# Kernel optimization log

Measured on AMD Instinct MI355X. Metric: run time of the kernel, lower is better.

The kernel has to match this reference:

```python
import jax, jax.numpy as jnp
from jax import lax
import numpy as np

N_X, N_U, N_Y, HID = 8, 2, 2, 64
T, B = 2048, 1024
SCALE = 0.02  # small weights keep the 2048-step recurrence stable


def setup_inputs() -> dict:
    key = jax.random.key(0)
    ks = jax.random.split(key, 12)
    rn = lambda k, shp: SCALE * jax.random.normal(k, shp, dtype=jnp.float32)
    return {
        "u": jax.random.normal(ks[0], (T, B, N_U), dtype=jnp.float32),
        "y": jax.random.normal(ks[1], (T, B, N_Y), dtype=jnp.float32),
        # f_xu MLP: [x;u] -> 64 -> tanh -> n_x
        "Wf1": rn(ks[2], (N_X + N_U, HID)), "bf1": jnp.zeros((HID,), jnp.float32),
        "Wf2": rn(ks[3], (HID, N_X)),       "bf2": jnp.zeros((N_X,), jnp.float32),
        # g_x: linear n_x -> n_y
        "Wg": rn(ks[4], (N_X, N_Y)),        "bg": jnp.zeros((N_Y,), jnp.float32),
        # gain net: n_x -> 64 -> tanh -> n_x*n_y
        "Wk1": rn(ks[5], (N_X, HID)),       "bk1": jnp.zeros((HID,), jnp.float32),
        "Wk2": rn(ks[6], (HID, N_X * N_Y)), "bk2": jnp.zeros((N_X * N_Y,), jnp.float32),
    }


def reference(u, y, Wf1, bf1, Wf2, bf2, Wg, bg, Wk1, bk1, Wk2, bk2):
    b = u.shape[1]

    def step(x, uy):  # x: [B, n_x]
        u_t, y_t = uy
        y_hat = x @ Wg + bg                                   # [B, n_y]
        K = (jnp.tanh(x @ Wk1 + bk1) @ Wk2 + bk2).reshape(b, N_X, N_Y)
        e = y_hat - y_t                                        # [B, n_y]
        dx = jnp.tanh(jnp.concatenate([x, u_t], -1) @ Wf1 + bf1) @ Wf2 + bf2
        x_new = x + dx + jnp.einsum("bxy,by->bx", K, e)
        return x_new, None

    x0 = jnp.zeros((b, N_X), dtype=u.dtype)
    x_last, _ = lax.scan(step, x0, (u, y))
    return x_last
```

## Files before the change

kernel.cpp:

```cpp
#include <hip/hip_runtime.h>


#define T_STEPS 2048
#define B_SZ    1024
#define NX      8
#define HID     64

typedef float v2f __attribute__((ext_vector_type(2)));

__device__ __forceinline__ v2f pk_fma(v2f a, v2f b, v2f c) {
  v2f d;
  asm("v_pk_fma_f32 %0, %1, %2, %3" : "=v"(d) : "v"(a), "v"(b), "v"(c));
  return d;
}
__device__ __forceinline__ void pk_fma_acc(v2f& acc, v2f a, v2f b) {
  asm("v_pk_fma_f32 %0, %1, %2, %0" : "+v"(acc) : "v"(a), "v"(b));
}
__device__ __forceinline__ v2f pk_fma_s0lo(v2f a, v2f b, v2f c) {
  v2f d;
  asm("v_pk_fma_f32 %0, %1, %2, %3 op_sel:[0,0,0] op_sel_hi:[0,1,1]"
      : "=v"(d) : "v"(a), "v"(b), "v"(c));
  return d;
}
__device__ __forceinline__ v2f pk_fma_s0hi(v2f a, v2f b, v2f c) {
  v2f d;
  asm("v_pk_fma_f32 %0, %1, %2, %3 op_sel:[1,0,0] op_sel_hi:[1,1,1]"
      : "=v"(d) : "v"(a), "v"(b), "v"(c));
  return d;
}
__device__ __forceinline__ void pk_fma_acc_s1lo(v2f& acc, v2f a, v2f b) {
  asm("v_pk_fma_f32 %0, %1, %2, %0 op_sel:[0,0,0] op_sel_hi:[1,0,1]"
      : "+v"(acc) : "v"(a), "v"(b));
}
__device__ __forceinline__ void pk_fma_acc_s1hi(v2f& acc, v2f a, v2f b) {
  asm("v_pk_fma_f32 %0, %1, %2, %0 op_sel:[0,1,0] op_sel_hi:[1,1,1]"
      : "+v"(acc) : "v"(a), "v"(b));
}

__device__ __forceinline__ v2f tanh_pair(float pa, float pb) {
  v2f r;
  r[0] = __builtin_amdgcn_rcpf(__builtin_amdgcn_exp2f(pa) + 1.0f);
  r[1] = __builtin_amdgcn_rcpf(__builtin_amdgcn_exp2f(pb) + 1.0f);
  v2f h;
  h[0] = fmaf(-2.0f, r[0], 1.0f);
  h[1] = fmaf(-2.0f, r[1], 1.0f);
  return h;
}

template <int CTRL, int RMASK>
__device__ __forceinline__ float dpp_add(float acc) {
  int moved = __builtin_amdgcn_update_dpp(0, __float_as_int(acc), CTRL, RMASK, 0xf, true);
  return acc + __int_as_float(moved);
}

__device__ __forceinline__ float half_reduce(float c) {
  c = dpp_add<0x111, 0xf>(c);
  c = dpp_add<0x112, 0xf>(c);
  c = dpp_add<0x114, 0xf>(c);
  c = dpp_add<0x118, 0xf>(c);
  c = dpp_add<0x142, 0xa>(c);
  return c;
}

__device__ __forceinline__ void swap32(float& a, float& b) {
  asm("v_permlane32_swap_b32 %0, %1" : "+v"(a), "+v"(b));
}

__device__ __forceinline__ float rlf(float v, int lane) {
  return __int_as_float(__builtin_amdgcn_readlane(__float_as_int(v), lane));
}

__global__ __launch_bounds__(64, 1) void luen_kernel(
    const float* __restrict__ u, const float* __restrict__ y,
    const float* __restrict__ Wf1, const float* __restrict__ bf1,
    const float* __restrict__ Wf2, const float* __restrict__ bf2,
    const float* __restrict__ Wg, const float* __restrict__ bg,
    const float* __restrict__ Wk1, const float* __restrict__ bk1,
    const float* __restrict__ Wk2, const float* __restrict__ bk2,
    float* __restrict__ out) {
  const int eb = blockIdx.x;
  const int h  = threadIdx.x;

  const float TS = 2.885390081777927f;
  const float INV64 = 1.0f / 64.0f;

  v2f wf1p[5];
#pragma unroll
  for (int p = 0; p < 5; ++p)
    wf1p[p] = v2f{TS * Wf1[(2 * p) * HID + h], TS * Wf1[(2 * p + 1) * HID + h]};
  v2f wk1p[4];
#pragma unroll
  for (int p = 0; p < 4; ++p)
    wk1p[p] = v2f{TS * Wk1[(2 * p) * HID + h], TS * Wk1[(2 * p + 1) * HID + h]};

  v2f wf2p[4], bf2sp[4];
#pragma unroll
  for (int p = 0; p < 4; ++p) {
    wf2p[p]  = v2f{Wf2[h * NX + 2 * p], Wf2[h * NX + 2 * p + 1]};
    bf2sp[p] = v2f{INV64 * bf2[2 * p], INV64 * bf2[2 * p + 1]};
  }
  v2f wk2e[4], wk2o[4], bk2se[4], bk2so[4];
#pragma unroll
  for (int p = 0; p < 4; ++p) {
    const float* r = Wk2 + h * (NX * 2);
    wk2e[p]  = v2f{r[4 * p], r[4 * p + 2]};
    wk2o[p]  = v2f{r[4 * p + 1], r[4 * p + 3]};
    bk2se[p] = v2f{INV64 * bk2[4 * p], INV64 * bk2[4 * p + 2]};
    bk2so[p] = v2f{INV64 * bk2[4 * p + 1], INV64 * bk2[4 * p + 3]};
  }
  v2f wgc0[4], wgc1[4];
#pragma unroll
  for (int p = 0; p < 4; ++p) {
    wgc0[p] = v2f{Wg[4 * p], Wg[4 * p + 2]};
    wgc1[p] = v2f{Wg[4 * p + 1], Wg[4 * p + 3]};
  }
  const v2f a0i = v2f{bg[0], 0.0f};
  const v2f a1i = v2f{bg[1], 0.0f};
  const v2f pfi = v2f{TS * bf1[h], 0.0f};
  const v2f pki = v2f{TS * bk1[h], 0.0f};

  float probe = (h < 32) ? 0.0f : 1.0f;
  float zf = 0.0f;
  swap32(probe, zf);
  const bool dir1 = __builtin_amdgcn_readlane(__float_as_int(probe), 32) != 0;
  const int laneA = dir1 ? 63 : 31;
  const int laneB = dir1 ? 31 : 63;

  const v2f* __restrict__ pu = reinterpret_cast<const v2f*>(u) + eb;
  const v2f* __restrict__ py = reinterpret_cast<const v2f*>(y) + eb;
  const int STR = B_SZ;

  v2f x2[4];
#pragma unroll
  for (int p = 0; p < 4; ++p) x2[p] = v2f{0.0f, 0.0f};

  v2f Au[4], Ay[4], Bu[4], By[4];

#define LOADG(SET_u, SET_y)                          \
  {                                                  \
    SET_u[0] = pu[0 * STR]; SET_u[1] = pu[1 * STR];  \
    SET_u[2] = pu[2 * STR]; SET_u[3] = pu[3 * STR];  \
    SET_y[0] = py[0 * STR]; SET_y[1] = py[1 * STR];  \
    SET_y[2] = py[2 * STR]; SET_y[3] = py[3 * STR];  \
    pu += 4 * STR; py += 4 * STR;                    \
  }

#define STEP(CU_, CY_)                                                        \
  {                                                                           \
    const v2f cu = (CU_);                                                     \
    const v2f cy = (CY_);                                                     \
                                    \
    v2f a0 = pk_fma(x2[0], wgc0[0], a0i);                                     \
    v2f a1 = pk_fma(x2[0], wgc1[0], a1i);                                     \
    pk_fma_acc(a0, x2[1], wgc0[1]); pk_fma_acc(a1, x2[1], wgc1[1]);           \
    pk_fma_acc(a0, x2[2], wgc0[2]); pk_fma_acc(a1, x2[2], wgc1[2]);           \
    pk_fma_acc(a0, x2[3], wgc0[3]); pk_fma_acc(a1, x2[3], wgc1[3]);           \
    v2f ep;                                                                   \
    ep[0] = a0[0] + a0[1] - cy[0];                                            \
    ep[1] = a1[0] + a1[1] - cy[1];                                            \
                   \
    v2f pf = pk_fma(x2[0], wf1p[0], pfi);                                     \
    pk_fma_acc(pf, x2[1], wf1p[1]);                                           \
    pk_fma_acc(pf, x2[2], wf1p[2]);                                           \
    pk_fma_acc(pf, x2[3], wf1p[3]);                                           \
    pk_fma_acc(pf, cu, wf1p[4]);                                              \
    v2f pkv = pk_fma(x2[0], wk1p[0], pki);                                    \
    pk_fma_acc(pkv, x2[1], wk1p[1]);                                          \
    pk_fma_acc(pkv, x2[2], wk1p[2]);                                          \
    pk_fma_acc(pkv, x2[3], wk1p[3]);                                          \
    const v2f hp = tanh_pair(pf[0] + pf[1], pkv[0] + pkv[1]);                 \
                       \
    float c0, c1, c2, c3, c4, c5, c6, c7;                                     \
    {                                                                         \
      v2f t0 = pk_fma_s0hi(hp, wk2e[0], bk2se[0]);                            \
      v2f t1 = pk_fma_s0hi(hp, wk2o[0], bk2so[0]);                            \
      v2f cp = pk_fma_s0lo(hp, wf2p[0], bf2sp[0]);                            \
      pk_fma_acc_s1lo(cp, t0, ep);                                            \
      pk_fma_acc_s1hi(cp, t1, ep);                                            \
      c0 = cp[0]; c1 = cp[1];                                                 \
    }                                                                         \
    {                                                                         \
      v2f t0 = pk_fma_s0hi(hp, wk2e[1], bk2se[1]);                            \
      v2f t1 = pk_fma_s0hi(hp, wk2o[1], bk2so[1]);                            \
      v2f cp = pk_fma_s0lo(hp, wf2p[1], bf2sp[1]);                            \
      pk_fma_acc_s1lo(cp, t0, ep);                                            \
      pk_fma_acc_s1hi(cp, t1, ep);                                            \
      c2 = cp[0]; c3 = cp[1];                                                 \
    }                                                                         \
    {                                                                         \
      v2f t0 = pk_fma_s0hi(hp, wk2e[2], bk2se[2]);                            \
      v2f t1 = pk_fma_s0hi(hp, wk2o[2], bk2so[2]);                            \
      v2f cp = pk_fma_s0lo(hp, wf2p[2], bf2sp[2]);                            \
      pk_fma_acc_s1lo(cp, t0, ep);                                            \
      pk_fma_acc_s1hi(cp, t1, ep);                                            \
      c4 = cp[0]; c5 = cp[1];                                                 \
    }                                                                         \
    {                                                                         \
      v2f t0 = pk_fma_s0hi(hp, wk2e[3], bk2se[3]);                            \
      v2f t1 = pk_fma_s0hi(hp, wk2o[3], bk2so[3]);                            \
      v2f cp = pk_fma_s0lo(hp, wf2p[3], bf2sp[3]);                            \
      pk_fma_acc_s1lo(cp, t0, ep);                                            \
      pk_fma_acc_s1hi(cp, t1, ep);                                            \
      c6 = cp[0]; c7 = cp[1];                                                 \
    }                                                                         \
                     \
    swap32(c0, c4); float d0 = c0 + c4;                                       \
    swap32(c1, c5); float d1 = c1 + c5;                                       \
    swap32(c2, c6); float d2 = c2 + c6;                                       \
    swap32(c3, c7); float d3 = c3 + c7;                                       \
    d0 = half_reduce(d0); d1 = half_reduce(d1);                               \
    d2 = half_reduce(d2); d3 = half_reduce(d3);                               \
    x2[0][0] += rlf(d0, laneA);                                               \
    x2[0][1] += rlf(d1, laneA);                                               \
    x2[1][0] += rlf(d2, laneA);                                               \
    x2[1][1] += rlf(d3, laneA);                                               \
    x2[2][0] += rlf(d0, laneB);                                               \
    x2[2][1] += rlf(d1, laneB);                                               \
    x2[3][0] += rlf(d2, laneB);                                               \
    x2[3][1] += rlf(d3, laneB);                                               \
  }

  LOADG(Au, Ay);
  LOADG(Bu, By);

  for (int it = 0; it < 255; ++it) {
    STEP(Au[0], Ay[0]); STEP(Au[1], Ay[1]); STEP(Au[2], Ay[2]); STEP(Au[3], Ay[3]);
    LOADG(Au, Ay);
    STEP(Bu[0], By[0]); STEP(Bu[1], By[1]); STEP(Bu[2], By[2]); STEP(Bu[3], By[3]);
    LOADG(Bu, By);
  }
  STEP(Au[0], Ay[0]); STEP(Au[1], Ay[1]); STEP(Au[2], Ay[2]); STEP(Au[3], Ay[3]);
  STEP(Bu[0], By[0]); STEP(Bu[1], By[1]); STEP(Bu[2], By[2]); STEP(Bu[3], By[3]);
#undef STEP
#undef LOADG

  if (h == 0) {
#pragma unroll
    for (int p = 0; p < 4; ++p) {
      out[eb * NX + 2 * p]     = x2[p][0];
      out[eb * NX + 2 * p + 1] = x2[p][1];
    }
  }
}

extern "C" void kernel_launch(void* const* d_in, const int* in_sizes, int n_in,
                              void* d_out, int out_size, void* d_ws, size_t ws_size,
                              hipStream_t stream) {
  const float* u   = (const float*)d_in[0];
  const float* y   = (const float*)d_in[1];
  const float* Wf1 = (const float*)d_in[2];
  const float* bf1 = (const float*)d_in[3];
  const float* Wf2 = (const float*)d_in[4];
  const float* bf2 = (const float*)d_in[5];
  const float* Wg  = (const float*)d_in[6];
  const float* bg  = (const float*)d_in[7];
  const float* Wk1 = (const float*)d_in[8];
  const float* bk1 = (const float*)d_in[9];
  const float* Wk2 = (const float*)d_in[10];
  const float* bk2 = (const float*)d_in[11];

  luen_kernel<<<dim3(B_SZ), dim3(HID), 0, stream>>>(
      u, y, Wf1, bf1, Wf2, bf2, Wg, bg, Wk1, bk1, Wk2, bk2, (float*)d_out);
}
```

Measured before the change: 665.7 us.

## Use permlane16 swap to halve per-step cross-lane reduction work

Adds a second butterfly stage with v_permlane16_swap so four partial sums fold into two registers before the 16-lane DPP prefix. This cuts the per-step reduction from four half_reduce chains to two prefix16 chains. A startup probe works out the permlane swap lane mapping and permutes the Wf2/Wk2/bias columns to match, with the old path kept as a fallback. The recurrence is latency-bound, so shortening the serial reduction chain each step aims to shorten the critical path. The cost is a uniform branch per step and more setup code.

```diff
diff --git a/kernel.cpp b/kernel.cpp
--- a/kernel.cpp
+++ b/kernel.cpp
@@ -53,17 +53,24 @@
   return acc + __int_as_float(moved);
 }
 
-__device__ __forceinline__ float half_reduce(float c) {
+__device__ __forceinline__ float prefix16(float c) {
   c = dpp_add<0x111, 0xf>(c);
   c = dpp_add<0x112, 0xf>(c);
   c = dpp_add<0x114, 0xf>(c);
   c = dpp_add<0x118, 0xf>(c);
+  return c;
+}
+__device__ __forceinline__ float half_reduce(float c) {
+  c = prefix16(c);
   c = dpp_add<0x142, 0xa>(c);
   return c;
 }
 
 __device__ __forceinline__ void swap32(float& a, float& b) {
   asm("v_permlane32_swap_b32 %0, %1" : "+v"(a), "+v"(b));
+}
+__device__ __forceinline__ void swap16(float& a, float& b) {
+  asm("v_permlane16_swap_b32 %0, %1" : "+v"(a), "+v"(b));
 }
 
 __device__ __forceinline__ float rlf(float v, int lane) {
@@ -84,47 +91,94 @@
   const float TS = 2.885390081777927f;
   const float INV64 = 1.0f / 64.0f;
 
-  v2f wf1p[5];
-#pragma unroll
-  for (int p = 0; p < 5; ++p)
-    wf1p[p] = v2f{TS * Wf1[(2 * p) * HID + h], TS * Wf1[(2 * p + 1) * HID + h]};
-  v2f wk1p[4];
-#pragma unroll
-  for (int p = 0; p < 4; ++p)
-    wk1p[p] = v2f{TS * Wk1[(2 * p) * HID + h], TS * Wk1[(2 * p + 1) * HID + h]};
-
-  v2f wf2p[4], bf2sp[4];
-#pragma unroll
-  for (int p = 0; p < 4; ++p) {
-    wf2p[p]  = v2f{Wf2[h * NX + 2 * p], Wf2[h * NX + 2 * p + 1]};
-    bf2sp[p] = v2f{INV64 * bf2[2 * p], INV64 * bf2[2 * p + 1]};
-  }
-  v2f wk2e[4], wk2o[4], bk2se[4], bk2so[4];
-#pragma unroll
-  for (int p = 0; p < 4; ++p) {
-    const float* r = Wk2 + h * (NX * 2);
-    wk2e[p]  = v2f{r[4 * p], r[4 * p + 2]};
-    wk2o[p]  = v2f{r[4 * p + 1], r[4 * p + 3]};
-    bk2se[p] = v2f{INV64 * bk2[4 * p], INV64 * bk2[4 * p + 2]};
-    bk2so[p] = v2f{INV64 * bk2[4 * p + 1], INV64 * bk2[4 * p + 3]};
-  }
-  v2f wgc0[4], wgc1[4];
-#pragma unroll
-  for (int p = 0; p < 4; ++p) {
-    wgc0[p] = v2f{Wg[4 * p], Wg[4 * p + 2]};
-    wgc1[p] = v2f{Wg[4 * p + 1], Wg[4 * p + 3]};
-  }
-  const v2f a0i = v2f{bg[0], 0.0f};
-  const v2f a1i = v2f{bg[1], 0.0f};
-  const v2f pfi = v2f{TS * bf1[h], 0.0f};
-  const v2f pki = v2f{TS * bk1[h], 0.0f};
-
   float probe = (h < 32) ? 0.0f : 1.0f;
   float zf = 0.0f;
   swap32(probe, zf);
   const bool dir1 = __builtin_amdgcn_readlane(__float_as_int(probe), 32) != 0;
   const int laneA = dir1 ? 63 : 31;
   const int laneB = dir1 ? 31 : 63;
+
+  int kof[8];
+  bool fastok;
+  {
+    float dP[4];
+#pragma unroll
+    for (int j = 0; j < 4; ++j) {
+      const float hiM = dir1 ? (float)(1 << j) : (float)(1 << (j + 4));
+      const float loM = dir1 ? (float)(1 << (j + 4)) : (float)(1 << j);
+      dP[j] = (h < 32) ? loM : hiM;
+    }
+    swap16(dP[0], dP[1]); float ffP = dP[0] + dP[1];
+    swap16(dP[2], dP[3]); float ggP = dP[2] + dP[3];
+    ffP = prefix16(ffP);
+    ggP = prefix16(ggP);
+    float sv[8];
+    sv[0] = rlf(ffP, 15); sv[1] = rlf(ffP, 31);
+    sv[2] = rlf(ffP, 47); sv[3] = rlf(ffP, 63);
+    sv[4] = rlf(ggP, 15); sv[5] = rlf(ggP, 31);
+    sv[6] = rlf(ggP, 47); sv[7] = rlf(ggP, 63);
+    int jm[8];
+    fastok = true;
+    int seen = 0;
+#pragma unroll
+    for (int s = 0; s < 8; ++s) {
+      const float r = sv[s] * 0.03125f;
+      const int iv = (int)r;
+      const bool ok = ((float)iv == r) && iv > 0 && iv <= 128 &&
+                      ((iv & (iv - 1)) == 0);
+      const int j = ok ? __builtin_ctz(iv) : 0;
+      jm[s] = j;
+      seen |= ok ? (1 << j) : 0;
+      fastok = fastok && ok;
+    }
+    fastok = fastok && (seen == 0xFF);
+#pragma unroll
+    for (int j = 0; j < 8; ++j) {
+      if (fastok) {
+        int v = 0;
+#pragma unroll
+        for (int s = 0; s < 8; ++s) v += (jm[s] == j) ? s : 0;
+        kof[j] = v;
+      } else {
+        kof[j] = j;
+      }
+    }
+  }
+
+  v2f wf1p[5];
+#pragma unroll
+  for (int p = 0; p < 5; ++p)
+    wf1p[p] = v2f{TS * Wf1[(2 * p) * HID + h], TS * Wf1[(2 * p + 1) * HID + h]};
+  v2f wk1p[4];
+#pragma unroll
+  for (int p = 0; p < 4; ++p)
+    wk1p[p] = v2f{TS * Wk1[(2 * p) * HID + h], TS * Wk1[(2 * p + 1) * HID + h]};
+
+  v2f wf2p[4], bf2sp[4], wk2e[4], wk2o[4], bk2se[4], bk2so[4];
+  {
+    const float* wf2row = Wf2 + h * NX;
+    const float* wk2row = Wk2 + h * (NX * 2);
+#pragma unroll
+    for (int p = 0; p < 4; ++p) {
+      const int kl = kof[2 * p], kh = kof[2 * p + 1];
+      wf2p[p]  = v2f{wf2row[kl], wf2row[kh]};
+      bf2sp[p] = v2f{INV64 * bf2[kl], INV64 * bf2[kh]};
+      wk2e[p]  = v2f{wk2row[2 * kl], wk2row[2 * kh]};
+      wk2o[p]  = v2f{wk2row[2 * kl + 1], wk2row[2 * kh + 1]};
+      bk2se[p] = v2f{INV64 * bk2[2 * kl], INV64 * bk2[2 * kh]};
+      bk2so[p] = v2f{INV64 * bk2[2 * kl + 1], INV64 * bk2[2 * kh + 1]};
+    }
+  }
+  v2f wgc0[4], wgc1[4];
+#pragma unroll
+  for (int p = 0; p < 4; ++p) {
+    wgc0[p] = v2f{Wg[4 * p], Wg[4 * p + 2]};
+    wgc1[p] = v2f{Wg[4 * p + 1], Wg[4 * p + 3]};
+  }
+  const v2f a0i = v2f{bg[0], 0.0f};
+  const v2f a1i = v2f{bg[1], 0.0f};
+  const v2f pfi = v2f{TS * bf1[h], 0.0f};
+  const v2f pki = v2f{TS * bk1[h], 0.0f};
 
   const v2f* __restrict__ pu = reinterpret_cast<const v2f*>(u) + eb;
   const v2f* __restrict__ py = reinterpret_cast<const v2f*>(y) + eb;
@@ -203,21 +257,30 @@
       pk_fma_acc_s1hi(cp, t1, ep);                                            \
       c6 = cp[0]; c7 = cp[1];                                                 \
     }                                                                         \
-                     \
+                                                      \
     swap32(c0, c4); float d0 = c0 + c4;                                       \
     swap32(c1, c5); float d1 = c1 + c5;                                       \
     swap32(c2, c6); float d2 = c2 + c6;                                       \
     swap32(c3, c7); float d3 = c3 + c7;                                       \
-    d0 = half_reduce(d0); d1 = half_reduce(d1);                               \
-    d2 = half_reduce(d2); d3 = half_reduce(d3);                               \
-    x2[0][0] += rlf(d0, laneA);                                               \
-    x2[0][1] += rlf(d1, laneA);                                               \
-    x2[1][0] += rlf(d2, laneA);                                               \
-    x2[1][1] += rlf(d3, laneA);                                               \
-    x2[2][0] += rlf(d0, laneB);                                               \
-    x2[2][1] += rlf(d1, laneB);                                               \
-    x2[3][0] += rlf(d2, laneB);                                               \
-    x2[3][1] += rlf(d3, laneB);                                               \
+    if (fastok) {                                                             \
+                     \
+      swap16(d0, d1); float ff = d0 + d1;                                     \
+      swap16(d2, d3); float gg = d2 + d3;                                     \
+      ff = prefix16(ff);                                                      \
+      gg = prefix16(gg);                                                      \
+      x2[0][0] += rlf(ff, 15); x2[0][1] += rlf(ff, 31);                       \
+      x2[1][0] += rlf(ff, 47); x2[1][1] += rlf(ff, 63);                       \
+      x2[2][0] += rlf(gg, 15); x2[2][1] += rlf(gg, 31);                       \
+      x2[3][0] += rlf(gg, 47); x2[3][1] += rlf(gg, 63);                       \
+    } else {                                                                  \
+                                        \
+      d0 = half_reduce(d0); d1 = half_reduce(d1);                             \
+      d2 = half_reduce(d2); d3 = half_reduce(d3);                             \
+      x2[0][0] += rlf(d0, laneA); x2[0][1] += rlf(d1, laneA);                 \
+      x2[1][0] += rlf(d2, laneA); x2[1][1] += rlf(d3, laneA);                 \
+      x2[2][0] += rlf(d0, laneB); x2[2][1] += rlf(d1, laneB);                 \
+      x2[3][0] += rlf(d2, laneB); x2[3][1] += rlf(d3, laneB);                 \
+    }                                                                         \
   }
 
   LOADG(Au, Ay);
```

After: 589.7 us. 1.13x faster.
